# Kernel optimization log

Measured on AMD Instinct MI355X. Metric: run time of the kernel, lower is better.

The kernel has to match this reference:

```python
import jax, jax.numpy as jnp
import numpy as np

P, T, L, K, N, K2, M, D = 16384, 8, 4096, 16, 2048, 32, 8, 64
ITER = 8
MM = {'flow_traffic': (0.0, 1e-4), 'flow_packets': (0.0, 1e-3), 'flow_packet_size': (0.0, 1e-3), 'link_capacity': (0.0, 1e-2)}


def _mlp2(x, w1, b1, w2, b2):
    return jax.nn.relu(jax.nn.relu(x @ w1 + b1) @ w2 + b2)


def _gru(x_proj, h, wh, bh):
    # Keras GRUCell, reset_after=True, gate order (z, r, h)
    hp = h @ wh + bh
    xz, xr, xc = jnp.split(x_proj, 3, axis=-1)
    hz, hr, hc = jnp.split(hp, 3, axis=-1)
    z = jax.nn.sigmoid(xz + hz)
    r = jax.nn.sigmoid(xr + hr)
    c = jnp.tanh(xc + r * hc)
    return z * h + (1.0 - z) * c


def setup_inputs() -> dict:
    key = jax.random.key(0)
    ks = iter(jax.random.split(key, 64))
    f32, i32 = jnp.float32, jnp.int32
    rn = lambda shape: jax.random.normal(next(ks), shape, dtype=f32) * 0.05
    inp = {}
    inp['flow_traffic'] = jax.random.uniform(next(ks), (P, 1), f32, 1.0, 1000.0)
    inp['flow_packets'] = jax.random.uniform(next(ks), (P, 1), f32, 1.0, 100.0)
    inp['flow_packet_size'] = jax.random.uniform(next(ks), (P, 1), f32, 64.0, 1500.0)
    inp['link_capacity'] = jax.random.uniform(next(ks), (L, 1), f32, 10.0, 100.0)
    inp['pe_w1'] = rn((3, D)); inp['pe_b1'] = jnp.zeros((D,), f32)
    inp['pe_w2'] = rn((D, D)); inp['pe_b2'] = jnp.zeros((D,), f32)
    inp['le_w1'] = rn((3, D)); inp['le_b1'] = jnp.zeros((D,), f32)
    inp['le_w2'] = rn((D, D)); inp['le_b2'] = jnp.zeros((D,), f32)
    inp['de_w1'] = rn((2, D)); inp['de_b1'] = jnp.zeros((D,), f32)
    inp['de_w2'] = rn((D, D)); inp['de_b2'] = jnp.zeros((D,), f32)
    for p in ('pgru', 'lgru', 'dgru'):
        inp[p + '_wx'] = rn((D, 3 * D)); inp[p + '_wh'] = rn((D, 3 * D))
        inp[p + '_bx'] = jnp.zeros((3 * D,), f32); inp[p + '_bh'] = jnp.zeros((3 * D,), f32)
    inp['ro_w1'] = rn((D, D // 2)); inp['ro_b1'] = jnp.zeros((D // 2,), f32)
    inp['ro_w2'] = rn((D // 2, D // 4)); inp['ro_b2'] = jnp.zeros((D // 4,), f32)
    inp['ro_w3'] = rn((D // 4, 1)); inp['ro_b3'] = jnp.zeros((1,), f32)
    inp['link_to_path'] = jax.random.randint(next(ks), (P, T), 0, L, i32)
    inp['node_to_path'] = jax.random.randint(next(ks), (P, T), 0, N, i32)
    inp['path_to_link'] = jnp.stack([jax.random.randint(next(ks), (L, K), 0, P, i32),
                                     jax.random.randint(next(ks), (L, K), 1, T + 1, i32)], axis=-1)
    inp['path_to_node'] = jnp.stack([jax.random.randint(next(ks), (N, K2), 0, P, i32),
                                     jax.random.randint(next(ks), (N, K2), 1, T + 1, i32)], axis=-1)
    inp['link_to_node'] = jax.random.randint(next(ks), (N, M), 0, L, i32)
    inp['nodes'] = jnp.zeros((N,), i32)
    inp['link_device_type'] = jnp.zeros((L,), i32)
    return inp


def reference(flow_traffic, flow_packets, flow_packet_size, link_capacity,
              pe_w1, pe_b1, pe_w2, pe_b2, le_w1, le_b1, le_w2, le_b2,
              de_w1, de_b1, de_w2, de_b2,
              pgru_wx, pgru_wh, pgru_bx, pgru_bh,
              lgru_wx, lgru_wh, lgru_bx, lgru_bh,
              dgru_wx, dgru_wh, dgru_bx, dgru_bh,
              ro_w1, ro_b1, ro_w2, ro_b2, ro_w3, ro_b3,
              link_to_path, node_to_path, path_to_link, path_to_node,
              link_to_node, nodes, link_device_type):
    # one_hot depth=1 -> 1.0 iff value==0
    ldt = (link_device_type == 0).astype(jnp.float32)[:, None]  # [L,1]
    # link load from path traffic
    load = flow_traffic[path_to_link[:, :, 0]].sum(axis=1) / (link_capacity * 1e9)  # [L,1]
    path_in = jnp.concatenate([
        (flow_traffic - MM['flow_traffic'][0]) * MM['flow_traffic'][1],
        (flow_packets - MM['flow_packets'][0]) * MM['flow_packets'][1],
        (flow_packet_size - MM['flow_packet_size'][0]) * MM['flow_packet_size'][1]], axis=1)
    path_state = _mlp2(path_in, pe_w1, pe_b1, pe_w2, pe_b2)  # [P,D]
    link_in = jnp.concatenate([(link_capacity - MM['link_capacity'][0]) * MM['link_capacity'][1], load, ldt], axis=1)
    link_state = _mlp2(link_in, le_w1, le_b1, le_w2, le_b2)  # [L,D]
    device_link_mean = link_state[link_to_node].sum(axis=1).mean(axis=1, keepdims=True)  # [N,1]
    devices_encoded = (nodes == 0).astype(jnp.float32)[:, None]  # [N,1]
    device_state = _mlp2(jnp.concatenate([devices_encoded, device_link_mean], axis=1),
                         de_w1, de_b1, de_w2, de_b2)  # [N,D]
    pl0, pl1 = path_to_link[:, :, 0], path_to_link[:, :, 1]
    pn0, pn1 = path_to_node[:, :, 0], path_to_node[:, :, 1]
    pss = None
    for _ in range(ITER):
        x = link_state[link_to_path] + device_state[node_to_path]  # [P,T,D]
        prev = path_state
        x_proj = jnp.swapaxes(x @ pgru_wx + pgru_bx, 0, 1)  # [T,P,3D]

        def step(h, xp):
            h2 = _gru(xp, h, pgru_wh, pgru_bh)
            return h2, h2

        path_state, seq = jax.lax.scan(step, path_state, x_proj)
        pss = jnp.concatenate([prev[:, None], jnp.swapaxes(seq, 0, 1)], axis=1)  # [P,T+1,D]
        link_state = _gru(pss[pl0, pl1].sum(axis=1) @ lgru_wx + lgru_bx, link_state, lgru_wh, lgru_bh)
        device_state = _gru(pss[pn0, pn1].sum(axis=1) @ dgru_wx + dgru_bx, device_state, dgru_wh, dgru_bh)
    h = jax.nn.relu(pss[:, 1:] @ ro_w1 + ro_b1)
    h = jax.nn.relu(h @ ro_w2 + ro_b2)
    occupancy = jax.nn.softplus(h @ ro_w3 + ro_b3)  # [P,T,1]
    delay = (occupancy / link_capacity[link_to_path]).sum(axis=1)  # [P,1]
    return delay
```

## Files before the change

kernel.cpp:

```cpp
#include <hip/hip_runtime.h>
#include <hip/hip_bf16.h>

static constexpr int PN = 16384;
static constexpr int TT = 8;
static constexpr int LN = 4096;
static constexpr int KG = 16;
static constexpr int NN = 2048;
static constexpr int K2G = 32;
static constexpr int MG = 8;
static constexpr int ITER = 8;

typedef __attribute__((ext_vector_type(8))) short short8b;
typedef __attribute__((ext_vector_type(4))) float f32x4;
typedef __attribute__((ext_vector_type(4))) unsigned int u32x4;

__device__ __forceinline__ float frcp(float x) {
    return __builtin_amdgcn_rcpf(x);
}
__device__ __forceinline__ float sigmoidf_(float x) {
    return frcp(1.0f + __expf(-x));
}
__device__ __forceinline__ float tanhf_(float x) {
    return 1.0f - 2.0f * frcp(__expf(2.0f * x) + 1.0f);
}
__device__ __forceinline__ float softplusf_(float x) {
    return fmaxf(x, 0.0f) + log1pf(__expf(-fabsf(x)));
}
__device__ __forceinline__ unsigned short f2bf(float f) {
    unsigned int x = __float_as_uint(f);
    unsigned int r = (x + 0x7fffu + ((x >> 16) & 1u)) >> 16;
    return (unsigned short)r;
}
__device__ __forceinline__ unsigned int pk2bf(float a, float b) {
    union { __hip_bfloat162 h; unsigned int u; } cvt;
    cvt.h = __float22bfloat162_rn(float2{a, b});
    return cvt.u;
}
__device__ __forceinline__ float bf2f(unsigned short u) {
    return __uint_as_float(((unsigned int)u) << 16);
}

__global__ __launch_bounds__(256) void k_setup(
    const float* __restrict__ ft, const float* __restrict__ fpk,
    const float* __restrict__ fps, const float* __restrict__ cap,
    const int* __restrict__ ptl, const int* __restrict__ ldt,
    const float* __restrict__ pe_w1, const float* __restrict__ pe_b1,
    const float* __restrict__ pe_w2, const float* __restrict__ pe_b2,
    const float* __restrict__ le_w1, const float* __restrict__ le_b1,
    const float* __restrict__ le_w2, const float* __restrict__ le_b2,
    const float* __restrict__ pgru_wx, const float* __restrict__ pgru_wh,
    const float* __restrict__ lgru_wx, const float* __restrict__ lgru_wh,
    const float* __restrict__ dgru_wx, const float* __restrict__ dgru_wh,
    unsigned short* __restrict__ pwxT, unsigned short* __restrict__ pwhT,
    unsigned short* __restrict__ lwxT, unsigned short* __restrict__ lwhT,
    unsigned short* __restrict__ dwxT, unsigned short* __restrict__ dwhT,
    float* __restrict__ path_state, float* __restrict__ link_state,
    unsigned short* __restrict__ lsb)
{
    int b = blockIdx.x;
    int tid = threadIdx.x;
    if (b >= 1280) {
        const float* srcs[6] = {pgru_wx, pgru_wh, lgru_wx, lgru_wh, dgru_wx, dgru_wh};
        unsigned short* dsts[6] = {pwxT, pwhT, lwxT, lwhT, dwxT, dwhT};
        int i = (b - 1280) * 256 + tid;
        int mi = i / 12288, o = i - mi * 12288;
        int n = o >> 6, k = o & 63;
        dsts[mi][o] = f2bf(srcs[mi][k * 192 + n]);
        return;
    }
    __shared__ __align__(16) float w2s[4096];
    __shared__ float w1s[192], b1s[64], b2s[64];
    __shared__ float h1s[4][64];
// ... 48 lines not shown
__global__ __launch_bounds__(256) void k_device_encode(
    const float* __restrict__ link_state, const int* __restrict__ ltn,
    const int* __restrict__ nodes,
    const float* __restrict__ w1, const float* __restrict__ b1,
    const float* __restrict__ w2, const float* __restrict__ b2,
    float* __restrict__ device_state, unsigned short* __restrict__ dsb)
{
    __shared__ __align__(16) float w2s[4096];
    __shared__ float h1s[4][64];
    int tid = threadIdx.x;
    for (int i = tid; i < 4096; i += 256) w2s[i] = w2[i];
    int rl = tid >> 6, d = tid & 63;
    int row = blockIdx.x * 4 + rl;
    float s = 0.0f;
#pragma unroll
    for (int m = 0; m < MG; ++m)
        s += link_state[(size_t)ltn[row * MG + m] * 64 + d];
#pragma unroll
    for (int o = 32; o > 0; o >>= 1) s += __shfl_xor(s, o);
    float dlm = s * (1.0f / 64.0f);
    float enc = (nodes[row] == 0) ? 1.0f : 0.0f;
    float h = b1[d] + enc * w1[d] + dlm * w1[64 + d];
    h1s[rl][d] = fmaxf(h, 0.0f);
    __syncthreads();
    float acc = b2[d];
#pragma unroll 8
    for (int k = 0; k < 64; ++k) acc += h1s[rl][k] * w2s[k * 64 + d];
    float v = fmaxf(acc, 0.0f);
    device_state[(size_t)row * 64 + d] = v;
    dsb[(size_t)row * 64 + d] = f2bf(v);
}

template <bool LAST>
__global__ __launch_bounds__(256, 4) void k_pscan(
    const unsigned short* __restrict__ lsb, const unsigned short* __restrict__ dsb,
    const int* __restrict__ ltp, const int* __restrict__ ntp,
    const unsigned short* __restrict__ wxT,
    const unsigned short* __restrict__ whT,
    const float* __restrict__ bx, const float* __restrict__ bh,
    float* __restrict__ path_state, unsigned short* __restrict__ pssb,
    const float* __restrict__ rw1, const float* __restrict__ rb1,
    const float* __restrict__ rw2, const float* __restrict__ rb2,
    const float* __restrict__ rw3, const float* __restrict__ rb3,
    const float* __restrict__ cap, float* __restrict__ out)
{
    __shared__ __align__(16) unsigned short Xs[8][16][72];
    __shared__ __align__(16) unsigned short Hb0[16][72];
    __shared__ int sIdx[256];
    __shared__ __align__(16) float rw1s[LAST ? 2048 : 4];
    __shared__ __align__(16) float rw2s[LAST ? 512 : 4];
    __shared__ float rw3s[16], rb1s[32], rb2s[16];
    int tid = threadIdx.x;
    int p0 = blockIdx.x * 16;

    if (LAST) {
        for (int i = tid; i < 2048; i += 256) rw1s[i] = rw1[i];
        for (int i = tid; i < 512; i += 256) rw2s[i] = rw2[i];
        if (tid < 16) rw3s[tid] = rw3[tid];
        if (tid < 32) rb1s[tid] = rb1[tid];
        if (tid < 16) rb2s[tid] = rb2[tid];
    }
    {
        int pi = tid >> 1;
        int m = pi & 15, t = pi >> 4;
        int gi = (p0 + m) * TT + t;
        sIdx[tid] = (tid & 1) ? __builtin_nontemporal_load(ntp + gi)
                              : __builtin_nontemporal_load(ltp + gi);
    }
    __syncthreads();
    {
        int j = tid & 15;
        int g = tid >> 4;
        uint2 A[8], B[8];
#pragma unroll
        for (int ro = 0; ro < 8; ++ro) {
            int pi = ro * 16 + g;
            int il = sIdx[pi * 2];
            int in = sIdx[pi * 2 + 1];
            A[ro] = *(const uint2*)(lsb + (size_t)il * 64 + j * 4);
            B[ro] = *(const uint2*)(dsb + (size_t)in * 64 + j * 4);
        }
#pragma unroll
        for (int ro = 0; ro < 8; ++ro) {
            float a0 = bf2f((unsigned short)A[ro].x);
            float a1 = bf2f((unsigned short)(A[ro].x >> 16));
            float a2 = bf2f((unsigned short)A[ro].y);
            float a3 = bf2f((unsigned short)(A[ro].y >> 16));
            float b0 = bf2f((unsigned short)B[ro].x);
            float b1 = bf2f((unsigned short)(B[ro].x >> 16));
            float b2 = bf2f((unsigned short)B[ro].y);
            float b3 = bf2f((unsigned short)(B[ro].y >> 16));
            uint2 u;
            u.x = pk2bf(a0 + b0, a1 + b1);
            u.y = pk2bf(a2 + b2, a3 + b3);
            *(uint2*)&Xs[ro][g][j * 4] = u;
        }
    }

    int lane = tid & 63, w = tid >> 6;
    int c = lane & 15, q = lane >> 4;
    int d = 16 * w + c;
    short8b fx[3][2], fh[3][2];
#pragma unroll
    for (int g = 0; g < 3; ++g)
#pragma unroll
        for (int kt = 0; kt < 2; ++kt) {
            int off = (g * 64 + 16 * w + c) * 64 + kt * 32 + q * 8;
            fx[g][kt] = *(const short8b*)(wxT + off);
            fh[g][kt] = *(const short8b*)(whT + off);
        }
    float bz = bx[d] + bh[d];
    float br = bx[64 + d] + bh[64 + d];
    float bxc = bx[128 + d];
    float bhc = bh[128 + d];
    float hold[4];
#pragma unroll
    for (int r_ = 0; r_ < 4; ++r_) {
        hold[r_] = path_state[(size_t)(p0 + q * 4 + r_) * 64 + d];
        Hb0[q * 4 + r_][d] = f2bf(hold[r_]);
    }
    __syncthreads();

    short8b aXc0 = *(const short8b*)&Xs[0][c][q * 8];
    short8b aXc1 = *(const short8b*)&Xs[0][c][32 + q * 8];

    for (int t = 0; t < TT; ++t) {
        f32x4 ax[3], ah[3];
        ax[0] = (f32x4){bz, bz, bz, bz};
        ax[1] = (f32x4){br, br, br, br};
        ax[2] = (f32x4){bxc, bxc, bxc, bxc};
        ah[0] = (f32x4){0.f, 0.f, 0.f, 0.f};
        ah[1] = (f32x4){0.f, 0.f, 0.f, 0.f};
        ah[2] = (f32x4){bhc, bhc, bhc, bhc};
        const unsigned short* hsrc = (t == 0) ? &Hb0[0][0] : &Xs[t - 1][0][0];
        short8b aH0 = *(const short8b*)(hsrc + c * 72 + q * 8);
        short8b aH1 = *(const short8b*)(hsrc + c * 72 + 32 + q * 8);
#pragma unroll
        for (int g = 0; g < 3; ++g) {
            ax[g] = __builtin_amdgcn_mfma_f32_16x16x32_bf16(aXc0, fx[g][0], ax[g], 0, 0, 0);
            ax[g] = __builtin_amdgcn_mfma_f32_16x16x32_bf16(aXc1, fx[g][1], ax[g], 0, 0, 0);
            ah[g] = __builtin_amdgcn_mfma_f32_16x16x32_bf16(aH0, fh[g][0], ah[g], 0, 0, 0);
            ah[g] = __builtin_amdgcn_mfma_f32_16x16x32_bf16(aH1, fh[g][1], ah[g], 0, 0, 0);
        }
        if (t < TT - 1) {
            aXc0 = *(const short8b*)&Xs[t + 1][c][q * 8];
            aXc1 = *(const short8b*)&Xs[t + 1][c][32 + q * 8];
        }
#pragma unroll
        for (int r_ = 0; r_ < 4; ++r_) {
            float z  = sigmoidf_(ax[0][r_] + ah[0][r_]);
            float rr = sigmoidf_(ax[1][r_] + ah[1][r_]);
            float cc = tanhf_(ax[2][r_] + rr * ah[2][r_]);
            float hn = cc + z * (hold[r_] - cc);
            hold[r_] = hn;
            Xs[t][q * 4 + r_][d] = f2bf(hn);
        }
        __syncthreads();
    }
    if (!LAST) {
#pragma unroll
        for (int r_ = 0; r_ < 4; ++r_)
            path_state[(size_t)(p0 + q * 4 + r_) * 64 + d] = hold[r_];
        {
            unsigned short* base = pssb + (size_t)p0 * TT * 64;
#pragma unroll
            for (int j = 0; j < 4; ++j) {
                int o = j * 2048 + tid * 8;
                int r = o >> 6;
                int c0 = o & 63;
                int m = r >> 3, t = r & 7;
                u32x4 v = *(const u32x4*)&Xs[t][m][c0];
                __builtin_nontemporal_store(v, (u32x4*)(base + o));
            }
        }
        return;
    }
    {
        int r = tid >> 1, hh = tid & 1;
        int m = r >> 3, t = r & 7;
        short8b rowv[8];
#pragma unroll
        for (int j = 0; j < 8; ++j)
            rowv[j] = *(const short8b*)&Xs[t][m][j * 8];
        float a1[16];
#pragma unroll
        for (int i = 0; i < 16; ++i) a1[i] = 0.f;
#pragma unroll 4
        for (int k = 0; k < 64; ++k) {
            float x = bf2f((unsigned short)rowv[k >> 3][k & 7]);
            const float* wr = &rw1s[k * 32 + hh * 16];
            float4 wa = *(const float4*)(wr);
            float4 wb = *(const float4*)(wr + 4);
            float4 wc = *(const float4*)(wr + 8);
            float4 wd = *(const float4*)(wr + 12);
            a1[0]  += x * wa.x; a1[1]  += x * wa.y; a1[2]  += x * wa.z; a1[3]  += x * wa.w;
            a1[4]  += x * wb.x; a1[5]  += x * wb.y; a1[6]  += x * wb.z; a1[7]  += x * wb.w;
            a1[8]  += x * wc.x; a1[9]  += x * wc.y; a1[10] += x * wc.z; a1[11] += x * wc.w;
            a1[12] += x * wd.x; a1[13] += x * wd.y; a1[14] += x * wd.z; a1[15] += x * wd.w;
        }
#pragma unroll
        for (int i = 0; i < 16; ++i)
            a1[i] = fmaxf(a1[i] + rb1s[hh * 16 + i], 0.0f);
        float h1[32];
#pragma unroll
        for (int i = 0; i < 16; ++i) {
            float o = __shfl_xor(a1[i], 1);
            h1[hh * 16 + i] = a1[i];
            h1[(1 - hh) * 16 + i] = o;
        }
        float a2[8];
#pragma unroll
        for (int i = 0; i < 8; ++i) a2[i] = 0.f;
#pragma unroll 4
        for (int k = 0; k < 32; ++k) {
            float x = h1[k];
            const float* wr = &rw2s[k * 16 + hh * 8];
            float4 wa = *(const float4*)(wr);
            float4 wb = *(const float4*)(wr + 4);
            a2[0] += x * wa.x; a2[1] += x * wa.y; a2[2] += x * wa.z; a2[3] += x * wa.w;
            a2[4] += x * wb.x; a2[5] += x * wb.y; a2[6] += x * wb.z; a2[7] += x * wb.w;
        }
#pragma unroll
        for (int i = 0; i < 8; ++i)
            a2[i] = fmaxf(a2[i] + rb2s[hh * 8 + i], 0.0f);
        float h2[16];
#pragma unroll
        for (int i = 0; i < 8; ++i) {
            float o = __shfl_xor(a2[i], 1);
            h2[hh * 8 + i] = a2[i];
            h2[(1 - hh) * 8 + i] = o;
        }
        float a3 = rb3[0];
#pragma unroll
        for (int k = 0; k < 16; ++k) a3 += h2[k] * rw3s[k];
        float occ = softplusf_(a3);
        float dcon = occ * frcp(cap[ltp[(p0 + m) * TT + t]]);
        float s = dcon;
        s += __shfl_xor(s, 2);
        s += __shfl_xor(s, 4);
        s += __shfl_xor(s, 8);
        if ((tid & 15) == 0) out[p0 + m] = s;
    }
}

template <int Kg>
__device__ __forceinline__ void edge_body(
    const unsigned short* __restrict__ wxT, const unsigned short* __restrict__ whT,
    const float* __restrict__ bx, const float* __restrict__ bh,
    const int* __restrict__ p2e, const unsigned short* __restrict__ pssb,
    float* __restrict__ state, unsigned short* __restrict__ smir, int blk)
{
    __shared__ int idxs[16 * Kg * 2];
    __shared__ __align__(16) unsigned short Ab[16][72];
    __shared__ __align__(16) unsigned short Hbs[16][72];
    __shared__ __align__(16) float Hf[16][68];
    int tid = threadIdx.x;
    int r0 = blk * 16;
    for (int i = tid; i < 16 * Kg * 2; i += 256)
        idxs[i] = p2e[(size_t)r0 * Kg * 2 + i];
    __syncthreads();
    {
        int r = tid >> 4, c4 = (tid & 15) * 4;
        int row = r0 + r;
        float4 s = {0.f, 0.f, 0.f, 0.f};
#pragma unroll
        for (int k = 0; k < Kg; ++k) {
            int pi = idxs[(r * Kg + k) * 2];
            int ti = idxs[(r * Kg + k) * 2 + 1];
            ushort4 v = *(const ushort4*)(pssb + ((size_t)pi * TT + ti - 1) * 64 + c4);
// ... 47 lines not shown
    for (int r = 0; r < 4; ++r) {
        int m = q * 4 + r;
        float z  = sigmoidf_(ax[0][r] + ah[0][r]);
        float rr = sigmoidf_(ax[1][r] + ah[1][r]);
        float cc = tanhf_(ax[2][r] + rr * ah[2][r]);
        float hn = cc + z * (Hf[m][d] - cc);
        state[(size_t)(r0 + m) * 64 + d] = hn;
        smir[(size_t)(r0 + m) * 64 + d] = f2bf(hn);
    }
}

__global__ __launch_bounds__(256) void k_edge_merged(
    const unsigned short* __restrict__ lwxT, const unsigned short* __restrict__ lwhT,
    const float* __restrict__ lbx, const float* __restrict__ lbh,
    const int* __restrict__ ptl,
    const unsigned short* __restrict__ dwxT, const unsigned short* __restrict__ dwhT,
    const float* __restrict__ dbx, const float* __restrict__ dbh,
    const int* __restrict__ ptn,
    const unsigned short* __restrict__ pssb,
    float* __restrict__ link_state, float* __restrict__ device_state,
    unsigned short* __restrict__ lsb, unsigned short* __restrict__ dsb)
{
    int b = blockIdx.x;
    if (b < LN / 16) {
        edge_body<KG>(lwxT, lwhT, lbx, lbh, ptl, pssb, link_state, lsb, b);
    } else {
        edge_body<K2G>(dwxT, dwhT, dbx, dbh, ptn, pssb, device_state, dsb, b - LN / 16);
    }
}

extern "C" void kernel_launch(void* const* d_in, const int* in_sizes, int n_in,
                              void* d_out, int out_size, void* d_ws, size_t ws_size,
                              hipStream_t stream) {
    const float* ft   = (const float*)d_in[0];
    const float* fpk  = (const float*)d_in[1];
    const float* fps  = (const float*)d_in[2];
    const float* cap  = (const float*)d_in[3];
    const float* pe_w1 = (const float*)d_in[4];
    const float* pe_b1 = (const float*)d_in[5];
    const float* pe_w2 = (const float*)d_in[6];
    const float* pe_b2 = (const float*)d_in[7];
    const float* le_w1 = (const float*)d_in[8];
    const float* le_b1 = (const float*)d_in[9];
    const float* le_w2 = (const float*)d_in[10];
    const float* le_b2 = (const float*)d_in[11];
    const float* de_w1 = (const float*)d_in[12];
    const float* de_b1 = (const float*)d_in[13];
    const float* de_w2 = (const float*)d_in[14];
    const float* de_b2 = (const float*)d_in[15];
    const float* pgru_wx = (const float*)d_in[16];
    const float* pgru_wh = (const float*)d_in[17];
    const float* pgru_bx = (const float*)d_in[18];
    const float* pgru_bh = (const float*)d_in[19];
    const float* lgru_wx = (const float*)d_in[20];
    const float* lgru_wh = (const float*)d_in[21];
    const float* lgru_bx = (const float*)d_in[22];
    const float* lgru_bh = (const float*)d_in[23];
    const float* dgru_wx = (const float*)d_in[24];
    const float* dgru_wh = (const float*)d_in[25];
    const float* dgru_bx = (const float*)d_in[26];
    const float* dgru_bh = (const float*)d_in[27];
    const float* ro_w1 = (const float*)d_in[28];
    const float* ro_b1 = (const float*)d_in[29];
    const float* ro_w2 = (const float*)d_in[30];
    const float* ro_b2 = (const float*)d_in[31];
    const float* ro_w3 = (const float*)d_in[32];
    const float* ro_b3 = (const float*)d_in[33];
    const int* ltp   = (const int*)d_in[34];
    const int* ntp   = (const int*)d_in[35];
    const int* ptl   = (const int*)d_in[36];
    const int* ptn   = (const int*)d_in[37];
    const int* ltn   = (const int*)d_in[38];
    const int* nodes = (const int*)d_in[39];
    const int* ldt   = (const int*)d_in[40];
    float* out = (float*)d_out;

    char* ws = (char*)d_ws;
    float* path_state = (float*)ws;      ws += (size_t)PN * 64 * 4;
    float* link_state = (float*)ws;      ws += (size_t)LN * 64 * 4;
    float* device_state = (float*)ws;    ws += (size_t)NN * 64 * 4;
    unsigned short* pssb = (unsigned short*)ws; ws += (size_t)PN * TT * 64 * 2;
    unsigned short* lsb  = (unsigned short*)ws; ws += (size_t)LN * 64 * 2;
    unsigned short* dsb  = (unsigned short*)ws; ws += (size_t)NN * 64 * 2;
    unsigned short* pwxT = (unsigned short*)ws; ws += 192 * 64 * 2;
    unsigned short* pwhT = (unsigned short*)ws; ws += 192 * 64 * 2;
    unsigned short* lwxT = (unsigned short*)ws; ws += 192 * 64 * 2;
    unsigned short* lwhT = (unsigned short*)ws; ws += 192 * 64 * 2;
    unsigned short* dwxT = (unsigned short*)ws; ws += 192 * 64 * 2;
    unsigned short* dwhT = (unsigned short*)ws; ws += 192 * 64 * 2;

    k_setup<<<1568, 256, 0, stream>>>(ft, fpk, fps, cap, ptl, ldt,
                                      pe_w1, pe_b1, pe_w2, pe_b2,
                                      le_w1, le_b1, le_w2, le_b2,
                                      pgru_wx, pgru_wh, lgru_wx, lgru_wh,
                                      dgru_wx, dgru_wh,
                                      pwxT, pwhT, lwxT, lwhT, dwxT, dwhT,
                                      path_state, link_state, lsb);
    k_device_encode<<<NN / 4, 256, 0, stream>>>(link_state, ltn, nodes, de_w1,
                                                de_b1, de_w2, de_b2, device_state, dsb);
    for (int it = 0; it < ITER - 1; ++it) {
        k_pscan<false><<<PN / 16, 256, 0, stream>>>(
            lsb, dsb, ltp, ntp, pwxT, pwhT, pgru_bx, pgru_bh,
            path_state, pssb, ro_w1, ro_b1, ro_w2, ro_b2, ro_w3, ro_b3, cap, out);
        k_edge_merged<<<LN / 16 + NN / 16, 256, 0, stream>>>(
            lwxT, lwhT, lgru_bx, lgru_bh, ptl,
            dwxT, dwhT, dgru_bx, dgru_bh, ptn,
            pssb, link_state, device_state, lsb, dsb);
    }
    k_pscan<true><<<PN / 16, 256, 0, stream>>>(
        lsb, dsb, ltp, ntp, pwxT, pwhT, pgru_bx, pgru_bh,
        path_state, pssb, ro_w1, ro_b1, ro_w2, ro_b2, ro_w3, ro_b3, cap, out);
}
```

Baseline: 388.9 us.

## Fuse all stages into one persistent kernel with software grid barriers

Replaces the sequence of setup, device-encode, per-iteration path-scan and edge-update launches with one persistent kernel of 1024 blocks. Stages are separated by an atomic-counter grid barrier, and each block keeps its path GRU hidden state in registers across iterations, so path_state is not re-read per iteration. This removes roughly 16 kernel launch gaps and the associated global round-trips. The cost is that all blocks must be co-resident (checked via an occupancy query with a fallback path), plus barrier spin overhead and idle blocks during the edge phases.

```diff
diff --git a/kernel.cpp b/kernel.cpp
--- a/kernel.cpp
+++ b/kernel.cpp
@@ -38,6 +38,434 @@
 }
 __device__ __forceinline__ float bf2f(unsigned short u) {
     return __uint_as_float(((unsigned int)u) << 16);
+}
+
+__device__ __forceinline__ void gridbar(unsigned* cnt, unsigned* gen, unsigned nb) {
+    __syncthreads();
+    if (threadIdx.x == 0) {
+        __threadfence();
+        unsigned g = __hip_atomic_load(gen, __ATOMIC_ACQUIRE, __HIP_MEMORY_SCOPE_AGENT);
+        unsigned a = __hip_atomic_fetch_add(cnt, 1u, __ATOMIC_ACQ_REL, __HIP_MEMORY_SCOPE_AGENT);
+        if (a + 1u == nb) {
+            __hip_atomic_store(cnt, 0u, __ATOMIC_RELAXED, __HIP_MEMORY_SCOPE_AGENT);
+            __hip_atomic_store(gen, g + 1u, __ATOMIC_RELEASE, __HIP_MEMORY_SCOPE_AGENT);
+        } else {
+            unsigned cur;
+            do {
+                __builtin_amdgcn_s_sleep(2);
+                cur = __hip_atomic_load(gen, __ATOMIC_ACQUIRE, __HIP_MEMORY_SCOPE_AGENT);
+            } while (cur == g);
+        }
+        __threadfence();
+    }
+    __syncthreads();
+}
+
+struct KArgs {
+    const float *ft, *fpk, *fps, *cap;
+    const int *ldt;
+    const float *pe_w1, *pe_b1, *pe_w2, *pe_b2;
+    const float *le_w1, *le_b1, *le_w2, *le_b2;
+    const float *de_w1, *de_b1, *de_w2, *de_b2;
+    const float *pgru_wx, *pgru_wh, *pgru_bx, *pgru_bh;
+    const float *lgru_wx, *lgru_wh, *lgru_bx, *lgru_bh;
+    const float *dgru_wx, *dgru_wh, *dgru_bx, *dgru_bh;
+    const float *ro_w1, *ro_b1, *ro_w2, *ro_b2, *ro_w3, *ro_b3;
+    const int *ltp, *ntp, *ptl, *ptn, *ltn, *nodes;
+    float *out;
+    float *path_state, *link_state, *device_state;
+    unsigned short *pssb, *lsb, *dsb;
+    unsigned short *pwxT, *pwhT, *lwxT, *lwhT, *dwxT, *dwhT;
+    unsigned *bar_cnt, *bar_gen;
+};
+
+static constexpr int SMEM_BYTES = 32256;
+
+template <int Kg>
+__device__ __forceinline__ void edge_body_f(
+    char* smem, int tid,
+    const unsigned short* __restrict__ wxT, const unsigned short* __restrict__ whT,
+    const float* __restrict__ bx, const float* __restrict__ bh,
+    const int* __restrict__ p2e, const unsigned short* __restrict__ pssb,
+    float* __restrict__ state, unsigned short* __restrict__ smir, int blk)
+{
+    int* idxs = (int*)smem;
+    unsigned short (*Ab)[72]  = (unsigned short(*)[72])(smem + 4096);
+    unsigned short (*Hbs)[72] = (unsigned short(*)[72])(smem + 6400);
+    float (*Hf)[68] = (float(*)[68])(smem + 8704);
+    int r0 = blk * 16;
+    for (int i = tid; i < 16 * Kg * 2; i += 256)
+        idxs[i] = p2e[(size_t)r0 * Kg * 2 + i];
+    __syncthreads();
+    {
+        int r = tid >> 4, c4 = (tid & 15) * 4;
+        int row = r0 + r;
+        float4 s = {0.f, 0.f, 0.f, 0.f};
+#pragma unroll
+        for (int k = 0; k < Kg; ++k) {
+            int pi = idxs[(r * Kg + k) * 2];
+            int ti = idxs[(r * Kg + k) * 2 + 1];
+            ushort4 v = *(const ushort4*)(pssb + ((size_t)pi * TT + ti - 1) * 64 + c4);
+            s.x += bf2f(v.x); s.y += bf2f(v.y);
+            s.z += bf2f(v.z); s.w += bf2f(v.w);
+        }
+        uint2 ua;
+        ua.x = pk2bf(s.x, s.y); ua.y = pk2bf(s.z, s.w);
+        *(uint2*)&Ab[r][c4] = ua;
+        float4 hv = *(const float4*)(state + (size_t)row * 64 + c4);
+        *(float4*)&Hf[r][c4] = hv;
+        uint2 uh;
+        uh.x = pk2bf(hv.x, hv.y); uh.y = pk2bf(hv.z, hv.w);
+        *(uint2*)&Hbs[r][c4] = uh;
+    }
+    __syncthreads();
+    int lane = tid & 63, w = tid >> 6;
+    int c = lane & 15, q = lane >> 4;
+    int d = 16 * w + c;
+    short8b fx[3][2], fh[3][2];
+#pragma unroll
+    for (int g = 0; g < 3; ++g)
+#pragma unroll
+        for (int kt = 0; kt < 2; ++kt) {
+            int off = (g * 64 + 16 * w + c) * 64 + kt * 32 + q * 8;
+            fx[g][kt] = *(const short8b*)(wxT + off);
+            fh[g][kt] = *(const short8b*)(whT + off);
+        }
+    float bz = bx[d] + bh[d];
+    float br = bx[64 + d] + bh[64 + d];
+    float bxc = bx[128 + d];
+    float bhc = bh[128 + d];
+    f32x4 ax[3], ah[3];
+    ax[0] = (f32x4){bz, bz, bz, bz};
+    ax[1] = (f32x4){br, br, br, br};
+    ax[2] = (f32x4){bxc, bxc, bxc, bxc};
+    ah[0] = (f32x4){0.f, 0.f, 0.f, 0.f};
+    ah[1] = (f32x4){0.f, 0.f, 0.f, 0.f};
+    ah[2] = (f32x4){bhc, bhc, bhc, bhc};
+#pragma unroll
+    for (int kt = 0; kt < 2; ++kt) {
+        short8b aA = *(const short8b*)&Ab[c][kt * 32 + q * 8];
+        short8b aH = *(const short8b*)&Hbs[c][kt * 32 + q * 8];
+#pragma unroll
+        for (int g = 0; g < 3; ++g) {
+            ax[g] = __builtin_amdgcn_mfma_f32_16x16x32_bf16(aA, fx[g][kt], ax[g], 0, 0, 0);
+            ah[g] = __builtin_amdgcn_mfma_f32_16x16x32_bf16(aH, fh[g][kt], ah[g], 0, 0, 0);
+        }
+    }
+#pragma unroll
+    for (int r = 0; r < 4; ++r) {
+        int m = q * 4 + r;
+        float z  = sigmoidf_(ax[0][r] + ah[0][r]);
+        float rr = sigmoidf_(ax[1][r] + ah[1][r]);
+        float cc = tanhf_(ax[2][r] + rr * ah[2][r]);
+        float hn = cc + z * (Hf[m][d] - cc);
+        state[(size_t)(r0 + m) * 64 + d] = hn;
+        smir[(size_t)(r0 + m) * 64 + d] = f2bf(hn);
+    }
+}
+
+__global__ __launch_bounds__(256, 4) void k_fused(KArgs A)
+{
+    __shared__ __align__(16) char smem[SMEM_BYTES];
+    const int bid = blockIdx.x;
+    const int tid = threadIdx.x;
+    const int p0 = bid * 16;
+    const unsigned NB = gridDim.x;
+
+    const int lane = tid & 63, w = tid >> 6;
+    const int c = lane & 15, q = lane >> 4;
+    const int d = 16 * w + c;
+
+    float* w2s = (float*)smem;
+    float* w1s = (float*)(smem + 16384);
+    float* b1s = (float*)(smem + 17152);
+    float* b2s = (float*)(smem + 17408);
+    float (*h1s)[64] = (float(*)[64])(smem + 17664);
+
+    unsigned short (*Xs)[16][72] = (unsigned short(*)[16][72])smem;
+    unsigned short (*Hb0)[72]    = (unsigned short(*)[72])(smem + 18432);
+    int*   sIdx = (int*)(smem + 20736);
+    float* rw1s = (float*)(smem + 21760);
+    float* rw2s = (float*)(smem + 29952);
+    float* rw3s = (float*)(smem + 32000);
+    float* rb1s = (float*)(smem + 32064);
+    float* rb2s = (float*)(smem + 32192);
+
+    {
+        int pi = tid >> 1;
+        int m = pi & 15, t = pi >> 4;
+        int gi = (p0 + m) * TT + t;
+        sIdx[tid] = (tid & 1) ? A.ntp[gi] : A.ltp[gi];
+        for (int i = tid; i < 2048; i += 256) rw1s[i] = A.ro_w1[i];
+        for (int i = tid; i < 512; i += 256) rw2s[i] = A.ro_w2[i];
+        if (tid < 16) rw3s[tid] = A.ro_w3[tid];
+        if (tid < 32) rb1s[tid] = A.ro_b1[tid];
+        if (tid < 16) rb2s[tid] = A.ro_b2[tid];
+    }
+
+    {
+        for (int i = tid; i < 4096; i += 256) w2s[i] = A.pe_w2[i];
+        if (tid < 192) w1s[tid] = A.pe_w1[tid];
+        if (tid < 64) { b1s[tid] = A.pe_b1[tid]; b2s[tid] = A.pe_b2[tid]; }
+        __syncthreads();
+        int rl = tid >> 6, dd = tid & 63;
+        for (int rp = 0; rp < 4; ++rp) {
+            int row = p0 + rp * 4 + rl;
+            float x0 = A.ft[row]  * 1e-4f;
+            float x1 = A.fpk[row] * 1e-3f;
+            float x2 = A.fps[row] * 1e-3f;
+            float h = b1s[dd] + x0 * w1s[dd] + x1 * w1s[64 + dd] + x2 * w1s[128 + dd];
+            h1s[rl][dd] = fmaxf(h, 0.0f);
+            __syncthreads();
+            float acc = b2s[dd];
+#pragma unroll 8
+            for (int k = 0; k < 64; ++k) acc += h1s[rl][k] * w2s[k * 64 + dd];
+            A.path_state[(size_t)row * 64 + dd] = fmaxf(acc, 0.0f);
+            __syncthreads();
+        }
+    }
+    if (bid < 256) {
+        for (int i = tid; i < 4096; i += 256) w2s[i] = A.le_w2[i];
+        if (tid < 192) w1s[tid] = A.le_w1[tid];
+        if (tid < 64) { b1s[tid] = A.le_b1[tid]; b2s[tid] = A.le_b2[tid]; }
+        __syncthreads();
+        int rl = tid >> 6, dd = tid & 63;
+        int base = bid * 16;
+        for (int rp = 0; rp < 4; ++rp) {
+            int row = base + rp * 4 + rl;
+            float v = 0.0f;
+            if (dd < 16) v = A.ft[A.ptl[(row * 16 + dd) * 2]];
+            v += __shfl_down(v, 8);
+            v += __shfl_down(v, 4);
+            v += __shfl_down(v, 2);
+            v += __shfl_down(v, 1);
+            float ssum = __shfl(v, 0);
+            float cv = A.cap[row];
+            float load = ssum * frcp(cv * 1e9f);
+            float x2 = (A.ldt[row] == 0) ? 1.0f : 0.0f;
+            float h = b1s[dd] + cv * 0.01f * w1s[dd] + load * w1s[64 + dd] + x2 * w1s[128 + dd];
+            h1s[rl][dd] = fmaxf(h, 0.0f);
+            __syncthreads();
+            float acc = b2s[dd];
+#pragma unroll 8
+            for (int k = 0; k < 64; ++k) acc += h1s[rl][k] * w2s[k * 64 + dd];
+            float vv = fmaxf(acc, 0.0f);
+            A.link_state[(size_t)row * 64 + dd] = vv;
+            A.lsb[(size_t)row * 64 + dd] = f2bf(vv);
+            __syncthreads();
+        }
+    }
+    if (bid >= 256 && bid < 544) {
+        const float* srcs[6] = {A.pgru_wx, A.pgru_wh, A.lgru_wx, A.lgru_wh, A.dgru_wx, A.dgru_wh};
+        unsigned short* dsts[6] = {A.pwxT, A.pwhT, A.lwxT, A.lwhT, A.dwxT, A.dwhT};
+        int i = (bid - 256) * 256 + tid;
+        int mi = i / 12288, o = i - mi * 12288;
+        int n = o >> 6, k = o & 63;
+        dsts[mi][o] = f2bf(srcs[mi][k * 192 + n]);
+    }
+    gridbar(A.bar_cnt, A.bar_gen, NB);
+
+    if (bid < 512) {
+        for (int i = tid; i < 4096; i += 256) w2s[i] = A.de_w2[i];
+        int rl = tid >> 6, dd = tid & 63;
+        int row = bid * 4 + rl;
+        float s = 0.0f;
+#pragma unroll
+        for (int m = 0; m < MG; ++m)
+            s += A.link_state[(size_t)A.ltn[row * MG + m] * 64 + dd];
+#pragma unroll
+        for (int o = 32; o > 0; o >>= 1) s += __shfl_xor(s, o);
+        float dlm = s * (1.0f / 64.0f);
+        float enc = (A.nodes[row] == 0) ? 1.0f : 0.0f;
+        float h = A.de_b1[dd] + enc * A.de_w1[dd] + dlm * A.de_w1[64 + dd];
+        h1s[rl][dd] = fmaxf(h, 0.0f);
+        __syncthreads();
+        float acc = A.de_b2[dd];
+#pragma unroll 8
+        for (int k = 0; k < 64; ++k) acc += h1s[rl][k] * w2s[k * 64 + dd];
+        float v = fmaxf(acc, 0.0f);
+        A.device_state[(size_t)row * 64 + dd] = v;
+        A.dsb[(size_t)row * 64 + dd] = f2bf(v);
+    }
+    gridbar(A.bar_cnt, A.bar_gen, NB);
+
+    const float bz  = A.pgru_bx[d] + A.pgru_bh[d];
+    const float brr = A.pgru_bx[64 + d] + A.pgru_bh[64 + d];
+    const float bxc = A.pgru_bx[128 + d];
+    const float bhc = A.pgru_bh[128 + d];
+    float hold[4];
+#pragma unroll
+    for (int r_ = 0; r_ < 4; ++r_)
+        hold[r_] = A.path_state[(size_t)(p0 + q * 4 + r_) * 64 + d];
+
+    for (int it = 0; it < ITER; ++it) {
+        const bool last = (it == ITER - 1);
+        {
+            int j = tid & 15;
+            int g = tid >> 4;
+            uint2 Av[8], Bv[8];
+#pragma unroll
+            for (int ro = 0; ro < 8; ++ro) {
+                int pi = ro * 16 + g;
+                int il = sIdx[pi * 2];
+                int in = sIdx[pi * 2 + 1];
+                Av[ro] = *(const uint2*)(A.lsb + (size_t)il * 64 + j * 4);
+                Bv[ro] = *(const uint2*)(A.dsb + (size_t)in * 64 + j * 4);
+            }
+#pragma unroll
+            for (int ro = 0; ro < 8; ++ro) {
+                float a0 = bf2f((unsigned short)Av[ro].x);
+                float a1 = bf2f((unsigned short)(Av[ro].x >> 16));
+                float a2 = bf2f((unsigned short)Av[ro].y);
+                float a3 = bf2f((unsigned short)(Av[ro].y >> 16));
+                float b0 = bf2f((unsigned short)Bv[ro].x);
+                float b1 = bf2f((unsigned short)(Bv[ro].x >> 16));
+                float b2 = bf2f((unsigned short)Bv[ro].y);
+                float b3 = bf2f((unsigned short)(Bv[ro].y >> 16));
+                uint2 u;
+                u.x = pk2bf(a0 + b0, a1 + b1);
+                u.y = pk2bf(a2 + b2, a3 + b3);
+                *(uint2*)&Xs[ro][g][j * 4] = u;
+            }
+        }
+        short8b fx[3][2], fh[3][2];
+#pragma unroll
+        for (int g = 0; g < 3; ++g)
+#pragma unroll
+            for (int kt = 0; kt < 2; ++kt) {
+                int off = (g * 64 + 16 * w + c) * 64 + kt * 32 + q * 8;
+                fx[g][kt] = *(const short8b*)(A.pwxT + off);
+                fh[g][kt] = *(const short8b*)(A.pwhT + off);
+            }
+#pragma unroll
+        for (int r_ = 0; r_ < 4; ++r_)
+            Hb0[q * 4 + r_][d] = f2bf(hold[r_]);
+        __syncthreads();
+
+        short8b aXc0 = *(const short8b*)&Xs[0][c][q * 8];
+        short8b aXc1 = *(const short8b*)&Xs[0][c][32 + q * 8];
+        for (int t = 0; t < TT; ++t) {
+            f32x4 ax[3], ah[3];
+            ax[0] = (f32x4){bz, bz, bz, bz};
+            ax[1] = (f32x4){brr, brr, brr, brr};
+            ax[2] = (f32x4){bxc, bxc, bxc, bxc};
+            ah[0] = (f32x4){0.f, 0.f, 0.f, 0.f};
+            ah[1] = (f32x4){0.f, 0.f, 0.f, 0.f};
+            ah[2] = (f32x4){bhc, bhc, bhc, bhc};
+            const unsigned short* hsrc = (t == 0) ? &Hb0[0][0] : &Xs[t - 1][0][0];
+            short8b aH0 = *(const short8b*)(hsrc + c * 72 + q * 8);
+            short8b aH1 = *(const short8b*)(hsrc + c * 72 + 32 + q * 8);
+#pragma unroll
+            for (int g = 0; g < 3; ++g) {
+                ax[g] = __builtin_amdgcn_mfma_f32_16x16x32_bf16(aXc0, fx[g][0], ax[g], 0, 0, 0);
+                ax[g] = __builtin_amdgcn_mfma_f32_16x16x32_bf16(aXc1, fx[g][1], ax[g], 0, 0, 0);
+                ah[g] = __builtin_amdgcn_mfma_f32_16x16x32_bf16(aH0, fh[g][0], ah[g], 0, 0, 0);
+                ah[g] = __builtin_amdgcn_mfma_f32_16x16x32_bf16(aH1, fh[g][1], ah[g], 0, 0, 0);
+            }
+            if (t < TT - 1) {
+                aXc0 = *(const short8b*)&Xs[t + 1][c][q * 8];
+                aXc1 = *(const short8b*)&Xs[t + 1][c][32 + q * 8];
+            }
+#pragma unroll
+            for (int r_ = 0; r_ < 4; ++r_) {
+                float z  = sigmoidf_(ax[0][r_] + ah[0][r_]);
+                float rr = sigmoidf_(ax[1][r_] + ah[1][r_]);
+                float cc = tanhf_(ax[2][r_] + rr * ah[2][r_]);
+                float hn = cc + z * (hold[r_] - cc);
+                hold[r_] = hn;
+                Xs[t][q * 4 + r_][d] = f2bf(hn);
+            }
+            __syncthreads();
+        }
+
+        if (!last) {
+            {
+                unsigned short* base = A.pssb + (size_t)p0 * TT * 64;
+#pragma unroll
+                for (int jj = 0; jj < 4; ++jj) {
+                    int o = jj * 2048 + tid * 8;
+                    int r = o >> 6;
+                    int c0 = o & 63;
+                    int m = r >> 3, t = r & 7;
+                    *(u32x4*)(base + o) = *(const u32x4*)&Xs[t][m][c0];
+                }
+            }
+            gridbar(A.bar_cnt, A.bar_gen, NB);
+            if (bid < LN / 16) {
+                edge_body_f<KG>(smem, tid, A.lwxT, A.lwhT, A.lgru_bx, A.lgru_bh,
+                                A.ptl, A.pssb, A.link_state, A.lsb, bid);
+            } else if (bid < LN / 16 + NN / 16) {
+                edge_body_f<K2G>(smem, tid, A.dwxT, A.dwhT, A.dgru_bx, A.dgru_bh,
+                                 A.ptn, A.pssb, A.device_state, A.dsb, bid - LN / 16);
+            }
+            gridbar(A.bar_cnt, A.bar_gen, NB);
+        } else {
+            int r = tid >> 1, hh = tid & 1;
+            int m = r >> 3, t = r & 7;
+            short8b rowv[8];
+#pragma unroll
+            for (int j = 0; j < 8; ++j)
+                rowv[j] = *(const short8b*)&Xs[t][m][j * 8];
+            float a1[16];
+#pragma unroll
+            for (int i = 0; i < 16; ++i) a1[i] = 0.f;
+#pragma unroll 4
+            for (int k = 0; k < 64; ++k) {
+                float x = bf2f((unsigned short)rowv[k >> 3][k & 7]);
+                const float* wr = &rw1s[k * 32 + hh * 16];
+                float4 wa = *(const float4*)(wr);
+                float4 wb = *(const float4*)(wr + 4);
+                float4 wc = *(const float4*)(wr + 8);
+                float4 wd = *(const float4*)(wr + 12);
+                a1[0]  += x * wa.x; a1[1]  += x * wa.y; a1[2]  += x * wa.z; a1[3]  += x * wa.w;
+                a1[4]  += x * wb.x; a1[5]  += x * wb.y; a1[6]  += x * wb.z; a1[7]  += x * wb.w;
+                a1[8]  += x * wc.x; a1[9]  += x * wc.y; a1[10] += x * wc.z; a1[11] += x * wc.w;
+                a1[12] += x * wd.x; a1[13] += x * wd.y; a1[14] += x * wd.z; a1[15] += x * wd.w;
+            }
+#pragma unroll
+            for (int i = 0; i < 16; ++i)
+                a1[i] = fmaxf(a1[i] + rb1s[hh * 16 + i], 0.0f);
+            float h1[32];
+#pragma unroll
+            for (int i = 0; i < 16; ++i) {
+                float o = __shfl_xor(a1[i], 1);
+                h1[hh * 16 + i] = a1[i];
+                h1[(1 - hh) * 16 + i] = o;
+            }
+            float a2[8];
+#pragma unroll
+            for (int i = 0; i < 8; ++i) a2[i] = 0.f;
+#pragma unroll 4
+            for (int k = 0; k < 32; ++k) {
+                float x = h1[k];
+                const float* wr = &rw2s[k * 16 + hh * 8];
+                float4 wa = *(const float4*)(wr);
+                float4 wb = *(const float4*)(wr + 4);
+                a2[0] += x * wa.x; a2[1] += x * wa.y; a2[2] += x * wa.z; a2[3] += x * wa.w;
+                a2[4] += x * wb.x; a2[5] += x * wb.y; a2[6] += x * wb.z; a2[7] += x * wb.w;
+            }
+#pragma unroll
+            for (int i = 0; i < 8; ++i)
+                a2[i] = fmaxf(a2[i] + rb2s[hh * 8 + i], 0.0f);
+            float h2[16];
+#pragma unroll
+            for (int i = 0; i < 8; ++i) {
+                float o = __shfl_xor(a2[i], 1);
+                h2[hh * 8 + i] = a2[i];
+                h2[(1 - hh) * 8 + i] = o;
+            }
+            float a3 = A.ro_b3[0];
+#pragma unroll
+            for (int k = 0; k < 16; ++k) a3 += h2[k] * rw3s[k];
+            float occ = softplusf_(a3);
+            float dcon = occ * frcp(A.cap[sIdx[(t * 16 + m) * 2]]);
+            float s = dcon;
+            s += __shfl_xor(s, 2);
+            s += __shfl_xor(s, 4);
+            s += __shfl_xor(s, 8);
+            if ((tid & 15) == 0) A.out[p0 + m] = s;
+        }
+    }
 }
 
 __global__ __launch_bounds__(256) void k_setup(
@@ -468,82 +896,98 @@
 extern "C" void kernel_launch(void* const* d_in, const int* in_sizes, int n_in,
                               void* d_out, int out_size, void* d_ws, size_t ws_size,
                               hipStream_t stream) {
-    const float* ft   = (const float*)d_in[0];
-    const float* fpk  = (const float*)d_in[1];
-    const float* fps  = (const float*)d_in[2];
-    const float* cap  = (const float*)d_in[3];
-    const float* pe_w1 = (const float*)d_in[4];
-    const float* pe_b1 = (const float*)d_in[5];
-    const float* pe_w2 = (const float*)d_in[6];
-    const float* pe_b2 = (const float*)d_in[7];
-    const float* le_w1 = (const float*)d_in[8];
-    const float* le_b1 = (const float*)d_in[9];
-    const float* le_w2 = (const float*)d_in[10];
-    const float* le_b2 = (const float*)d_in[11];
-    const float* de_w1 = (const float*)d_in[12];
-    const float* de_b1 = (const float*)d_in[13];
-    const float* de_w2 = (const float*)d_in[14];
-    const float* de_b2 = (const float*)d_in[15];
-    const float* pgru_wx = (const float*)d_in[16];
-    const float* pgru_wh = (const float*)d_in[17];
-    const float* pgru_bx = (const float*)d_in[18];
-    const float* pgru_bh = (const float*)d_in[19];
-    const float* lgru_wx = (const float*)d_in[20];
-    const float* lgru_wh = (const float*)d_in[21];
-    const float* lgru_bx = (const float*)d_in[22];
-    const float* lgru_bh = (const float*)d_in[23];
-    const float* dgru_wx = (const float*)d_in[24];
-    const float* dgru_wh = (const float*)d_in[25];
-    const float* dgru_bx = (const float*)d_in[26];
-    const float* dgru_bh = (const float*)d_in[27];
-    const float* ro_w1 = (const float*)d_in[28];
-    const float* ro_b1 = (const float*)d_in[29];
-    const float* ro_w2 = (const float*)d_in[30];
-    const float* ro_b2 = (const float*)d_in[31];
-    const float* ro_w3 = (const float*)d_in[32];
-    const float* ro_b3 = (const float*)d_in[33];
-    const int* ltp   = (const int*)d_in[34];
-    const int* ntp   = (const int*)d_in[35];
-    const int* ptl   = (const int*)d_in[36];
-    const int* ptn   = (const int*)d_in[37];
-    const int* ltn   = (const int*)d_in[38];
-    const int* nodes = (const int*)d_in[39];
-    const int* ldt   = (const int*)d_in[40];
-    float* out = (float*)d_out;
+    KArgs A;
+    A.ft    = (const float*)d_in[0];
+    A.fpk   = (const float*)d_in[1];
+    A.fps   = (const float*)d_in[2];
+    A.cap   = (const float*)d_in[3];
+    A.pe_w1 = (const float*)d_in[4];
+    A.pe_b1 = (const float*)d_in[5];
+    A.pe_w2 = (const float*)d_in[6];
+    A.pe_b2 = (const float*)d_in[7];
+    A.le_w1 = (const float*)d_in[8];
+    A.le_b1 = (const float*)d_in[9];
+    A.le_w2 = (const float*)d_in[10];
+    A.le_b2 = (const float*)d_in[11];
+    A.de_w1 = (const float*)d_in[12];
+    A.de_b1 = (const float*)d_in[13];
+    A.de_w2 = (const float*)d_in[14];
+    A.de_b2 = (const float*)d_in[15];
+    A.pgru_wx = (const float*)d_in[16];
+    A.pgru_wh = (const float*)d_in[17];
+    A.pgru_bx = (const float*)d_in[18];
+    A.pgru_bh = (const float*)d_in[19];
+    A.lgru_wx = (const float*)d_in[20];
+    A.lgru_wh = (const float*)d_in[21];
+    A.lgru_bx = (const float*)d_in[22];
+    A.lgru_bh = (const float*)d_in[23];
+    A.dgru_wx = (const float*)d_in[24];
+    A.dgru_wh = (const float*)d_in[25];
+    A.dgru_bx = (const float*)d_in[26];
+    A.dgru_bh = (const float*)d_in[27];
+    A.ro_w1 = (const float*)d_in[28];
+    A.ro_b1 = (const float*)d_in[29];
+    A.ro_w2 = (const float*)d_in[30];
+    A.ro_b2 = (const float*)d_in[31];
+    A.ro_w3 = (const float*)d_in[32];
+    A.ro_b3 = (const float*)d_in[33];
+    A.ltp   = (const int*)d_in[34];
+    A.ntp   = (const int*)d_in[35];
+    A.ptl   = (const int*)d_in[36];
+    A.ptn   = (const int*)d_in[37];
+    A.ltn   = (const int*)d_in[38];
+    A.nodes = (const int*)d_in[39];
+    A.ldt   = (const int*)d_in[40];
+    A.out   = (float*)d_out;
 
     char* ws = (char*)d_ws;
-    float* path_state = (float*)ws;      ws += (size_t)PN * 64 * 4;
-    float* link_state = (float*)ws;      ws += (size_t)LN * 64 * 4;
-    float* device_state = (float*)ws;    ws += (size_t)NN * 64 * 4;
-    unsigned short* pssb = (unsigned short*)ws; ws += (size_t)PN * TT * 64 * 2;
-    unsigned short* lsb  = (unsigned short*)ws; ws += (size_t)LN * 64 * 2;
-    unsigned short* dsb  = (unsigned short*)ws; ws += (size_t)NN * 64 * 2;
-    unsigned short* pwxT = (unsigned short*)ws; ws += 192 * 64 * 2;
-    unsigned short* pwhT = (unsigned short*)ws; ws += 192 * 64 * 2;
-    unsigned short* lwxT = (unsigned short*)ws; ws += 192 * 64 * 2;
-    unsigned short* lwhT = (unsigned short*)ws; ws += 192 * 64 * 2;
-    unsigned short* dwxT = (unsigned short*)ws; ws += 192 * 64 * 2;
-    unsigned short* dwhT = (unsigned short*)ws; ws += 192 * 64 * 2;
-
-    k_setup<<<1568, 256, 0, stream>>>(ft, fpk, fps, cap, ptl, ldt,
-                                      pe_w1, pe_b1, pe_w2, pe_b2,
-                                      le_w1, le_b1, le_w2, le_b2,
-                                      pgru_wx, pgru_wh, lgru_wx, lgru_wh,
-                                      dgru_wx, dgru_wh,
-                                      pwxT, pwhT, lwxT, lwhT, dwxT, dwhT,
-                                      path_state, link_state, lsb);
-    k_device_encode<<<NN / 4, 256, 0, stream>>>(link_state, ltn, nodes, de_w1,
-                                                de_b1, de_w2, de_b2, device_state, dsb);
+    A.path_state = (float*)ws;      ws += (size_t)PN * 64 * 4;
+    A.link_state = (float*)ws;      ws += (size_t)LN * 64 * 4;
+    A.device_state = (float*)ws;    ws += (size_t)NN * 64 * 4;
+    A.pssb = (unsigned short*)ws;   ws += (size_t)PN * TT * 64 * 2;
+    A.lsb  = (unsigned short*)ws;   ws += (size_t)LN * 64 * 2;
+    A.dsb  = (unsigned short*)ws;   ws += (size_t)NN * 64 * 2;
+    A.pwxT = (unsigned short*)ws;   ws += 192 * 64 * 2;
+    A.pwhT = (unsigned short*)ws;   ws += 192 * 64 * 2;
+    A.lwxT = (unsigned short*)ws;   ws += 192 * 64 * 2;
+    A.lwhT = (unsigned short*)ws;   ws += 192 * 64 * 2;
+    A.dwxT = (unsigned short*)ws;   ws += 192 * 64 * 2;
+    A.dwhT = (unsigned short*)ws;   ws += 192 * 64 * 2;
+    A.bar_cnt = (unsigned*)ws;      ws += sizeof(unsigned);
+    A.bar_gen = (unsigned*)ws;      ws += sizeof(unsigned);
+
+    int maxb = 0;
+    hipError_t qerr = hipOccupancyMaxActiveBlocksPerMultiprocessor(&maxb, k_fused, 256, 0);
+    bool use_fused = (qerr == hipSuccess && maxb >= 4);
+
+    if (use_fused) {
+        hipMemsetAsync(A.bar_cnt, 0, 2 * sizeof(unsigned), stream);
+        k_fused<<<PN / 16, 256, 0, stream>>>(A);
+        return;
+    }
+
+    k_setup<<<1568, 256, 0, stream>>>(A.ft, A.fpk, A.fps, A.cap, A.ptl, A.ldt,
+                                      A.pe_w1, A.pe_b1, A.pe_w2, A.pe_b2,
+                                      A.le_w1, A.le_b1, A.le_w2, A.le_b2,
+                                      A.pgru_wx, A.pgru_wh, A.lgru_wx, A.lgru_wh,
+                                      A.dgru_wx, A.dgru_wh,
+                                      A.pwxT, A.pwhT, A.lwxT, A.lwhT, A.dwxT, A.dwhT,
+                                      A.path_state, A.link_state, A.lsb);
+    k_device_encode<<<NN / 4, 256, 0, stream>>>(A.link_state, A.ltn, A.nodes, A.de_w1,
+                                                A.de_b1, A.de_w2, A.de_b2,
+                                                A.device_state, A.dsb);
     for (int it = 0; it < ITER - 1; ++it) {
         k_pscan<false><<<PN / 16, 256, 0, stream>>>(
-            lsb, dsb, ltp, ntp, pwxT, pwhT, pgru_bx, pgru_bh,
-            path_state, pssb, ro_w1, ro_b1, ro_w2, ro_b2, ro_w3, ro_b3, cap, out);
+            A.lsb, A.dsb, A.ltp, A.ntp, A.pwxT, A.pwhT, A.pgru_bx, A.pgru_bh,
+            A.path_state, A.pssb, A.ro_w1, A.ro_b1, A.ro_w2, A.ro_b2, A.ro_w3,
+            A.ro_b3, A.cap, A.out);
         k_edge_merged<<<LN / 16 + NN / 16, 256, 0, stream>>>(
-            lwxT, lwhT, lgru_bx, lgru_bh, ptl,
-            dwxT, dwhT, dgru_bx, dgru_bh, ptn,
-            pssb, link_state, device_state, lsb, dsb);
+            A.lwxT, A.lwhT, A.lgru_bx, A.lgru_bh, A.ptl,
+            A.dwxT, A.dwhT, A.dgru_bx, A.dgru_bh, A.ptn,
+            A.pssb, A.link_state, A.device_state, A.lsb, A.dsb);
     }
     k_pscan<true><<<PN / 16, 256, 0, stream>>>(
-        lsb, dsb, ltp, ntp, pwxT, pwhT, pgru_bx, pgru_bh,
-        path_state, pssb, ro_w1, ro_b1, ro_w2, ro_b2, ro_w3, ro_b3, cap, out);
-}
+        A.lsb, A.dsb, A.ltp, A.ntp, A.pwxT, A.pwhT, A.pgru_bx, A.pgru_bh,
+        A.path_state, A.pssb, A.ro_w1, A.ro_b1, A.ro_w2, A.ro_b2, A.ro_w3,
+        A.ro_b3, A.cap, A.out);
+}
```

Result: no change. 385.3 us (-0.9%).

## Halve paths per pscan block to double grid size and raise occupancy

Applied to the files above, without the earlier changes.

The path-GRU scan kernel now handles 8 paths per block instead of 16. This doubles the grid, and the non-last variant gets a higher occupancy hint in launch bounds. Because the 16-row MFMA tiles are now only half filled, the extra rows are padded by duplicating path p0. The initial hidden-state fragment is built straight from global fp32 memory instead of an Hb0 shared buffer, and the readout reuses the shared link indices to look up capacity. The aim is more parallelism and wavefronts in flight for the latency-bound recurrent scan, at the cost of wasting half the matrix-core work and reloading the weight fragments in twice as many blocks.

```diff
diff --git a/kernel.cpp b/kernel.cpp
--- a/kernel.cpp
+++ b/kernel.cpp
@@ -38,6 +38,14 @@
 }
 __device__ __forceinline__ float bf2f(unsigned short u) {
     return __uint_as_float(((unsigned int)u) << 16);
+}
+__device__ __forceinline__ short8b frag2(float4 a, float4 b) {
+    union { short8b v; unsigned int u[4]; } r;
+    r.u[0] = pk2bf(a.x, a.y);
+    r.u[1] = pk2bf(a.z, a.w);
+    r.u[2] = pk2bf(b.x, b.y);
+    r.u[3] = pk2bf(b.z, b.w);
+    return r.v;
 }
 
 __global__ __launch_bounds__(256) void k_setup(
@@ -152,7 +160,7 @@
 }
 
 template <bool LAST>
-__global__ __launch_bounds__(256, 4) void k_pscan(
+__global__ __launch_bounds__(256, LAST ? 4 : 8) void k_pscan(
     const unsigned short* __restrict__ lsb, const unsigned short* __restrict__ dsb,
     const int* __restrict__ ltp, const int* __restrict__ ntp,
     const unsigned short* __restrict__ wxT,
@@ -165,13 +173,12 @@
     const float* __restrict__ cap, float* __restrict__ out)
 {
     __shared__ __align__(16) unsigned short Xs[8][16][72];
-    __shared__ __align__(16) unsigned short Hb0[16][72];
-    __shared__ int sIdx[256];
+    __shared__ int sIdx[128];
     __shared__ __align__(16) float rw1s[LAST ? 2048 : 4];
     __shared__ __align__(16) float rw2s[LAST ? 512 : 4];
     __shared__ float rw3s[16], rb1s[32], rb2s[16];
     int tid = threadIdx.x;
-    int p0 = blockIdx.x * 16;
+    int p0 = blockIdx.x * 8;
 
     if (LAST) {
         for (int i = tid; i < 2048; i += 256) rw1s[i] = rw1[i];
@@ -180,9 +187,9 @@
         if (tid < 32) rb1s[tid] = rb1[tid];
         if (tid < 16) rb2s[tid] = rb2[tid];
     }
-    {
+    if (tid < 128) {
         int pi = tid >> 1;
-        int m = pi & 15, t = pi >> 4;
+        int t = pi >> 3, m = pi & 7;
         int gi = (p0 + m) * TT + t;
         sIdx[tid] = (tid & 1) ? __builtin_nontemporal_load(ntp + gi)
                               : __builtin_nontemporal_load(ltp + gi);
@@ -191,9 +198,9 @@
     {
         int j = tid & 15;
         int g = tid >> 4;
-        uint2 A[8], B[8];
-#pragma unroll
-        for (int ro = 0; ro < 8; ++ro) {
+        uint2 A[4], B[4];
+#pragma unroll
+        for (int ro = 0; ro < 4; ++ro) {
             int pi = ro * 16 + g;
             int il = sIdx[pi * 2];
             int in = sIdx[pi * 2 + 1];
@@ -201,7 +208,9 @@
             B[ro] = *(const uint2*)(dsb + (size_t)in * 64 + j * 4);
         }
 #pragma unroll
-        for (int ro = 0; ro < 8; ++ro) {
+        for (int ro = 0; ro < 4; ++ro) {
+            int pi = ro * 16 + g;
+            int t = pi >> 3, m = pi & 7;
             float a0 = bf2f((unsigned short)A[ro].x);
             float a1 = bf2f((unsigned short)(A[ro].x >> 16));
             float a2 = bf2f((unsigned short)A[ro].y);
@@ -213,7 +222,7 @@
             uint2 u;
             u.x = pk2bf(a0 + b0, a1 + b1);
             u.y = pk2bf(a2 + b2, a3 + b3);
-            *(uint2*)&Xs[ro][g][j * 4] = u;
+            *(uint2*)&Xs[t][m][j * 4] = u;
         }
     }
 
@@ -236,8 +245,20 @@
     float hold[4];
 #pragma unroll
     for (int r_ = 0; r_ < 4; ++r_) {
-        hold[r_] = path_state[(size_t)(p0 + q * 4 + r_) * 64 + d];
-        Hb0[q * 4 + r_][d] = f2bf(hold[r_]);
+        int rowi = q * 4 + r_;
+        int prow = (rowi < 8) ? (p0 + rowi) : p0;
+        hold[r_] = path_state[(size_t)prow * 64 + d];
+    }
+    short8b aH0s, aH1s;
+    {
+        int pc = (c < 8) ? (p0 + c) : p0;
+        const float* hr = path_state + (size_t)pc * 64;
+        float4 a0 = *(const float4*)(hr + q * 8);
+        float4 a1 = *(const float4*)(hr + q * 8 + 4);
+        float4 a2 = *(const float4*)(hr + 32 + q * 8);
+        float4 a3 = *(const float4*)(hr + 32 + q * 8 + 4);
+        aH0s = frag2(a0, a1);
+        aH1s = frag2(a2, a3);
     }
     __syncthreads();
 
@@ -252,9 +273,13 @@
         ah[0] = (f32x4){0.f, 0.f, 0.f, 0.f};
         ah[1] = (f32x4){0.f, 0.f, 0.f, 0.f};
         ah[2] = (f32x4){bhc, bhc, bhc, bhc};
-        const unsigned short* hsrc = (t == 0) ? &Hb0[0][0] : &Xs[t - 1][0][0];
-        short8b aH0 = *(const short8b*)(hsrc + c * 72 + q * 8);
-        short8b aH1 = *(const short8b*)(hsrc + c * 72 + 32 + q * 8);
+        short8b aH0, aH1;
+        if (t == 0) { aH0 = aH0s; aH1 = aH1s; }
+        else {
+            const unsigned short* hsrc = &Xs[t - 1][0][0];
+            aH0 = *(const short8b*)(hsrc + c * 72 + q * 8);
+            aH1 = *(const short8b*)(hsrc + c * 72 + 32 + q * 8);
+        }
 #pragma unroll
         for (int g = 0; g < 3; ++g) {
             ax[g] = __builtin_amdgcn_mfma_f32_16x16x32_bf16(aXc0, fx[g][0], ax[g], 0, 0, 0);
@@ -278,24 +303,23 @@
         __syncthreads();
     }
     if (!LAST) {
-#pragma unroll
-        for (int r_ = 0; r_ < 4; ++r_)
-            path_state[(size_t)(p0 + q * 4 + r_) * 64 + d] = hold[r_];
+        if (q < 2) {
+#pragma unroll
+            for (int r_ = 0; r_ < 4; ++r_)
+                path_state[(size_t)(p0 + q * 4 + r_) * 64 + d] = hold[r_];
+        }
         {
             unsigned short* base = pssb + (size_t)p0 * TT * 64;
-#pragma unroll
-            for (int j = 0; j < 4; ++j) {
-                int o = j * 2048 + tid * 8;
-                int r = o >> 6;
-                int c0 = o & 63;
-                int m = r >> 3, t = r & 7;
-                u32x4 v = *(const u32x4*)&Xs[t][m][c0];
-                __builtin_nontemporal_store(v, (u32x4*)(base + o));
-            }
+            int o = tid * 16;
+            int r = o >> 6;
+            int c0 = o & 63;
+            int m = r >> 3, t = r & 7;
+            __builtin_nontemporal_store(*(const u32x4*)&Xs[t][m][c0], (u32x4*)(base + o));
+            __builtin_nontemporal_store(*(const u32x4*)&Xs[t][m][c0 + 8], (u32x4*)(base + o + 8));
         }
         return;
     }
-    {
+    if (tid < 128) {
         int r = tid >> 1, hh = tid & 1;
         int m = r >> 3, t = r & 7;
         short8b rowv[8];
@@ -354,7 +378,7 @@
 #pragma unroll
         for (int k = 0; k < 16; ++k) a3 += h2[k] * rw3s[k];
         float occ = softplusf_(a3);
-        float dcon = occ * frcp(cap[ltp[(p0 + m) * TT + t]]);
+        float dcon = occ * frcp(cap[sIdx[(t * 8 + m) * 2]]);
         float s = dcon;
         s += __shfl_xor(s, 2);
         s += __shfl_xor(s, 4);
@@ -535,7 +559,7 @@
     k_device_encode<<<NN / 4, 256, 0, stream>>>(link_state, ltn, nodes, de_w1,
                                                 de_b1, de_w2, de_b2, device_state, dsb);
     for (int it = 0; it < ITER - 1; ++it) {
-        k_pscan<false><<<PN / 16, 256, 0, stream>>>(
+        k_pscan<false><<<PN / 8, 256, 0, stream>>>(
             lsb, dsb, ltp, ntp, pwxT, pwhT, pgru_bx, pgru_bh,
             path_state, pssb, ro_w1, ro_b1, ro_w2, ro_b2, ro_w3, ro_b3, cap, out);
         k_edge_merged<<<LN / 16 + NN / 16, 256, 0, stream>>>(
@@ -543,7 +567,7 @@
             dwxT, dwhT, dgru_bx, dgru_bh, ptn,
             pssb, link_state, device_state, lsb, dsb);
     }
-    k_pscan<true><<<PN / 16, 256, 0, stream>>>(
+    k_pscan<true><<<PN / 8, 256, 0, stream>>>(
         lsb, dsb, ltp, ntp, pwxT, pwhT, pgru_bx, pgru_bh,
         path_state, pssb, ro_w1, ro_b1, ro_w2, ro_b2, ro_w3, ro_b3, cap, out);
 }
```

New measurement: 1.206 ms. 3.1x slower.
